# Optimization experiments

Measured on AMD Instinct MI355X. Metric: run time of the kernel, lower is better.

## Reference

```python
import jax, jax.numpy as jnp
import numpy as np

H, W = 128, 128
TANFOVX = 0.5
TANFOVY = 0.5
SCALE_MOD = 1.0
NEAR = 0.2
N = 2048


def setup_inputs() -> dict:
    key = jax.random.key(0)
    ks = jax.random.split(key, 6)
    # Gaussians in front of an identity camera looking down +z
    xy = jax.random.uniform(ks[0], (N, 2), minval=-1.5, maxval=1.5)
    z = jax.random.uniform(ks[1], (N, 1), minval=2.5, maxval=6.5)
    means3D = jnp.concatenate([xy, z], axis=1).astype(jnp.float32)
    opacities = jax.random.uniform(ks[2], (N, 1), minval=0.05, maxval=0.95)
    colors_precomp = jax.random.uniform(ks[3], (N, 3))
    scales = jax.random.uniform(ks[4], (N, 3), minval=0.01, maxval=0.06)
    rotations = jax.random.normal(ks[5], (N, 4))
    viewmatrix = jnp.eye(4, dtype=jnp.float32)  # world == camera frame
    bg = jnp.zeros((3,), dtype=jnp.float32)
    return dict(means3D=means3D, opacities=opacities,
                colors_precomp=colors_precomp, scales=scales,
                rotations=rotations, viewmatrix=viewmatrix, bg=bg)


def _quat_to_rot(q):
    # normalized quaternion (w, x, y, z) -> rotation matrix, as in the CUDA kernel
    q = q / jnp.linalg.norm(q, axis=-1, keepdims=True)
    w, x, y, z = q[:, 0], q[:, 1], q[:, 2], q[:, 3]
    return jnp.stack([
        jnp.stack([1 - 2 * (y * y + z * z), 2 * (x * y - w * z), 2 * (x * z + w * y)], -1),
        jnp.stack([2 * (x * y + w * z), 1 - 2 * (x * x + z * z), 2 * (y * z - w * x)], -1),
        jnp.stack([2 * (x * z - w * y), 2 * (y * z + w * x), 1 - 2 * (x * x + y * y)], -1),
    ], -2)  # [N,3,3]


def _forward(means3D, opacities, colors_precomp, scales, rotations, viewmatrix, bg):
    fx = W / (2.0 * TANFOVX)
    fy = H / (2.0 * TANFOVY)
    Rv = viewmatrix[:3, :3]
    tv = viewmatrix[:3, 3]
    pv = means3D @ Rv.T + tv            # view-space positions [N,3]
    x, y, z = pv[:, 0], pv[:, 1], pv[:, 2]
    zc = jnp.maximum(z, 1e-4)
    # frustum clamping of the EWA Jacobian, as in forward.cu
    tx = jnp.clip(x / zc, -1.3 * TANFOVX, 1.3 * TANFOVX) * zc
    ty = jnp.clip(y / zc, -1.3 * TANFOVY, 1.3 * TANFOVY) * zc
    zeros = jnp.zeros_like(zc)
    J = jnp.stack([
        jnp.stack([fx / zc, zeros, -fx * tx / (zc * zc)], -1),
        jnp.stack([zeros, fy / zc, -fy * ty / (zc * zc)], -1),
    ], -2)                               # [N,2,3]
    # 3D covariance Sigma = R S S^T R^T
    Rg = _quat_to_rot(rotations)
    M = Rg * (scales * SCALE_MOD)[:, None, :]
    Sigma = M @ jnp.swapaxes(M, -1, -2)  # [N,3,3]
    T2 = jnp.einsum('nij,jk->nik', J, Rv)
    cov2d = jnp.einsum('nij,njk,nlk->nil', T2, Sigma, T2)
    a = cov2d[:, 0, 0] + 0.3             # low-pass filter, as in CUDA
    b = cov2d[:, 0, 1]
    c = cov2d[:, 1, 1] + 0.3
    det = a * c - b * b
    valid = (det > 0) & (z > NEAR)
    inv_det = jnp.where(det != 0, 1.0 / det, 0.0)
    conA, conB, conC = c * inv_det, -b * inv_det, a * inv_det
    mid = 0.5 * (a + c)
    lam = mid + jnp.sqrt(jnp.maximum(mid * mid - det, 0.1))
    radii = jnp.where(valid, jnp.ceil(3.0 * jnp.sqrt(lam)), 0.0)
    # projected pixel-space means
    mx = fx * (x / zc) + 0.5 * (W - 1)
    my = fy * (y / zc) + 0.5 * (H - 1)

    # global front-to-back depth sort (CUDA sorts per tile; one tile here)
    order = jnp.argsort(z)
    mx_s, my_s = mx[order], my[order]
    A_s, B_s, C_s = conA[order], conB[order], conC[order]
    op_s = opacities[order, 0]
    z_s = z[order]
    col_s = colors_precomp[order]
    valid_s = valid[order]

    px = jnp.arange(W, dtype=means3D.dtype)
    py = jnp.arange(H, dtype=means3D.dtype)
    Dx = mx_s[None, :] - px[:, None]     # [W,N]
    Dy = my_s[None, :] - py[:, None]     # [H,N]
    # power = -0.5 (A dx^2 + C dy^2) - B dx dy, built [H,W,N]
    power = (-0.5 * A_s * Dx * Dx)[None, :, :] \
            + (-0.5 * C_s * Dy * Dy)[:, None, :] \
            - (B_s * Dx)[None, :, :] * Dy[:, None, :]
    alpha = jnp.minimum(0.99, op_s * jnp.exp(jnp.minimum(power, 0.0)))
    alpha = jnp.where((power <= 0.0) & valid_s & (alpha >= 1.0 / 255.0), alpha, 0.0)
    alpha = alpha.reshape(H * W, N)      # [HW,N], front-to-back order
    logt = jnp.log1p(-alpha)
    csum = jnp.cumsum(logt, axis=-1)
    T_excl = jnp.exp(csum - logt)        # exclusive transmittance prod_{j<i}(1-a_j)
    wgt = alpha * T_excl                 # compositing weights
    T_final = jnp.exp(csum[:, -1])
    color = jnp.einsum('pn,nc->cp', wgt, col_s).reshape(3, H, W) \
            + T_final.reshape(1, H, W) * bg[:, None, None]
    depth = (wgt * z_s[None, :]).sum(-1).reshape(H, W)
    alpha_img = (1.0 - T_final).reshape(H, W)
    return color, radii, depth, alpha_img


def reference(means3D, opacities, colors_precomp, scales, rotations, viewmatrix, bg):
    return _forward(means3D, opacities, colors_precomp, scales, rotations, viewmatrix, bg)
```

## Files before the change

### kernel.cpp

```cpp
#include <hip/hip_runtime.h>

#define NG    2048
#define IMG_W 128
#define IMG_H 128
#define NPIX  (IMG_W * IMG_H)
#define REC   12

__global__ __launch_bounds__(256) void prep_rank_kernel(
    const float* __restrict__ means,
    const float* __restrict__ opac,
    const float* __restrict__ cols,
    const float* __restrict__ scales,
    const float* __restrict__ rots,
    const float* __restrict__ vm4,
    float* __restrict__ s,
    float4* __restrict__ key4,
    float* __restrict__ radii_out)
{
    __shared__ __align__(16) float zl[NG];
    int tid = threadIdx.x;

    const double fx = 128.0, fy = 128.0;

    double R00 = vm4[0], R01 = vm4[1], R02 = vm4[2],  t0 = vm4[3];
    double R10 = vm4[4], R11 = vm4[5], R12 = vm4[6],  t1 = vm4[7];
    double R20 = vm4[8], R21 = vm4[9], R22 = vm4[10], t2 = vm4[11];

    for (int j = tid; j < NG; j += 256) {
        double zj = R20*means[3*j] + R21*means[3*j+1] + R22*means[3*j+2] + t2;
        zl[j] = (float)zj;
    }
    __syncthreads();

    int g = tid >> 4;
    int p = tid & 15;
    int i = blockIdx.x * 16 + g;
    float zi = zl[i];

    const float4* z4 = (const float4*)zl;
    int rank = 0;
    #pragma unroll 4
    for (int it = 0; it < 32; ++it) {
        int idx = it * 16 + p;
        float4 f = z4[idx];
        int j0 = idx * 4;
        rank += (f.x < zi) || (f.x == zi && (j0 + 0) < i);
        rank += (f.y < zi) || (f.y == zi && (j0 + 1) < i);
        rank += (f.z < zi) || (f.z == zi && (j0 + 2) < i);
        rank += (f.w < zi) || (f.w == zi && (j0 + 3) < i);
    }
    rank += __shfl_down(rank, 8, 16);
    rank += __shfl_down(rank, 4, 16);
    rank += __shfl_down(rank, 2, 16);
    rank += __shfl_down(rank, 1, 16);

    if (p != 0) return;

    double m0 = means[3*i+0], m1 = means[3*i+1], m2 = means[3*i+2];
    double x = R00*m0 + R01*m1 + R02*m2 + t0;
    double y = R10*m0 + R11*m1 + R12*m2 + t1;
    double z = R20*m0 + R21*m1 + R22*m2 + t2;

    double zc   = fmax(z, 1e-4);
    double invz = 1.0 / zc;
    const double limx = 1.3 * 0.5, limy = 1.3 * 0.5;
    double tx = fmin(limx, fmax(-limx, x * invz)) * zc;
    double ty = fmin(limy, fmax(-limy, y * invz)) * zc;

    double J00 = fx * invz, J02 = -fx * tx * invz * invz;
    double J11 = fy * invz, J12 = -fy * ty * invz * invz;

    double qw = rots[4*i+0], qx = rots[4*i+1], qy = rots[4*i+2], qz = rots[4*i+3];
    double qn = 1.0 / sqrt(qw*qw + qx*qx + qy*qy + qz*qz);
    qw *= qn; qx *= qn; qy *= qn; qz *= qn;

    double Rg00 = 1.0 - 2.0*(qy*qy + qz*qz), Rg01 = 2.0*(qx*qy - qw*qz), Rg02 = 2.0*(qx*qz + qw*qy);
    double Rg10 = 2.0*(qx*qy + qw*qz), Rg11 = 1.0 - 2.0*(qx*qx + qz*qz), Rg12 = 2.0*(qy*qz - qw*qx);
    double Rg20 = 2.0*(qx*qz - qw*qy), Rg21 = 2.0*(qy*qz + qw*qx), Rg22 = 1.0 - 2.0*(qx*qx + qy*qy);

    double s0 = scales[3*i+0], s1 = scales[3*i+1], s2 = scales[3*i+2];
    double M00 = Rg00*s0, M01 = Rg01*s1, M02 = Rg02*s2;
    double M10 = Rg10*s0, M11 = Rg11*s1, M12 = Rg12*s2;
    double M20 = Rg20*s0, M21 = Rg21*s1, M22 = Rg22*s2;

    double S00 = M00*M00 + M01*M01 + M02*M02;
    double S01 = M00*M10 + M01*M11 + M02*M12;
    double S02 = M00*M20 + M01*M21 + M02*M22;
    double S11 = M10*M10 + M11*M11 + M12*M12;
    double S12 = M10*M20 + M11*M21 + M12*M22;
    double S22 = M20*M20 + M21*M21 + M22*M22;

    double Ta0 = J00*R00 + J02*R20, Ta1 = J00*R01 + J02*R21, Ta2 = J00*R02 + J02*R22;
    double Tb0 = J11*R10 + J12*R20, Tb1 = J11*R11 + J12*R21, Tb2 = J11*R12 + J12*R22;

    double Ua0 = Ta0*S00 + Ta1*S01 + Ta2*S02;
    double Ua1 = Ta0*S01 + Ta1*S11 + Ta2*S12;
    double Ua2 = Ta0*S02 + Ta1*S12 + Ta2*S22;
    double Ub0 = Tb0*S00 + Tb1*S01 + Tb2*S02;
    double Ub1 = Tb0*S01 + Tb1*S11 + Tb2*S12;
    double Ub2 = Tb0*S02 + Tb1*S12 + Tb2*S22;
    double cov00 = Ua0*Ta0 + Ua1*Ta1 + Ua2*Ta2;
    double cov01 = Ua0*Tb0 + Ua1*Tb1 + Ua2*Tb2;
    double cov11 = Ub0*Tb0 + Ub1*Tb1 + Ub2*Tb2;

    double a = cov00 + 0.3;
    double b = cov01;
    double c = cov11 + 0.3;
    double det = a*c - b*b;
    bool valid = (det > 0.0) && (z > 0.2);
    double inv_det = (det != 0.0) ? (1.0 / det) : 0.0;
    double conA =  c * inv_det;
    double conB = -b * inv_det;
    double conC =  a * inv_det;
    double mid = 0.5 * (a + c);
    double lam = mid + sqrt(fmax(mid*mid - det, 0.1));
    float radii = valid ? (float)ceil(3.0 * sqrt(lam)) : 0.0f;

    double mx = fx * (x * invz) + 0.5 * (IMG_W - 1);
    double my = fy * (y * invz) + 0.5 * (IMG_H - 1);

    double op = valid ? (double)opac[i] : 0.0;

    double r2c = -1.0;
    if (op > 0.0) {
        double lnterm = log(255.0 * op);
        if (lnterm > 0.0) r2c = 2.0 * lnterm * lam * 1.0001 + 1e-3;
    }

    float* dst = s + (size_t)rank * REC;
    *(float4*)(dst)     = make_float4((float)mx, (float)my, (float)conA, (float)conB);
    *(float4*)(dst + 4) = make_float4((float)conC, (float)op, (float)z, cols[3*i+0]);
    *(float4*)(dst + 8) = make_float4(cols[3*i+1], cols[3*i+2], (float)r2c, 0.0f);
    key4[rank]   = make_float4((float)mx, (float)my, (float)r2c, 0.0f);
    radii_out[i] = radii;
}

__global__ __launch_bounds__(256) void composite_kernel(
    const float* __restrict__ s,
    const float4* __restrict__ key4,
    const float* __restrict__ bg,
    float* __restrict__ out)
{
    __shared__ float comb[4 * 64 * 5];

    int tid  = threadIdx.x;
    int lane = tid & 63;
    int w    = tid >> 6;
    int tile = blockIdx.x;
    int x0 = (tile & 15) * 8;
    int y0 = (tile >> 4) * 8;
    float x0f = (float)x0,       y0f = (float)y0;
    float x1f = (float)(x0 + 7), y1f = (float)(y0 + 7);

    int px = x0 + (lane & 7);
    int py = y0 + (lane >> 3);
    float fpx = (float)px, fpy = (float)py;
    int p = py * IMG_W + px;

    const int SEG = NG / 4;
    int segbase = w * SEG;

    unsigned long long m[8];
    unsigned pb = 0;
    #pragma unroll
    for (int c = 0; c < 8; ++c) {
        float4 k4 = key4[segbase + c * 64 + lane];
        float ddx = fmaxf(0.f, fmaxf(x0f - k4.x, k4.x - x1f));
        float ddy = fmaxf(0.f, fmaxf(y0f - k4.y, k4.y - y1f));
        bool pass = (ddx*ddx + ddy*ddy) <= k4.z;
        m[c] = __ballot(pass);
        pb |= pass ? (1u << c) : 0u;
    }

    float cr = 0.f, cg = 0.f, cb = 0.f, dep = 0.f, T = 1.f;

    #pragma unroll
    for (int c = 0; c < 8; ++c) {
        unsigned long long mm = m[c];
        if (!mm) continue;
        float4 a0 = make_float4(0.f,0.f,0.f,0.f);
        float4 a1 = a0;
        float2 a2 = make_float2(0.f,0.f);
        if ((pb >> c) & 1u) {
            const float* r = s + (size_t)(segbase + c * 64 + lane) * REC;
            a0 = *(const float4*)(r);
            a1 = *(const float4*)(r + 4);
            a2 = *(const float2*)(r + 8);
        }
        while (mm) {
            int b = __ffsll(mm) - 1;
            mm &= mm - 1;
            float mx = __shfl(a0.x, b);
            float my = __shfl(a0.y, b);
            float A  = __shfl(a0.z, b);
            float B  = __shfl(a0.w, b);
            float C  = __shfl(a1.x, b);
            float op = __shfl(a1.y, b);
            float dx = mx - fpx;
            float dy = my - fpy;
            float power = -0.5f * (A*dx*dx + C*dy*dy) - B*dx*dy;
            float al = fminf(0.99f, op * __expf(power));
            bool take = (power <= 0.0f) && (al >= (1.0f / 255.0f));
            if (__any(take)) {
                float gz = __shfl(a1.z, b);
                float gr = __shfl(a1.w, b);
                float gg = __shfl(a2.x, b);
                float gb = __shfl(a2.y, b);
                float wgt = take ? al * T : 0.0f;
                dep += wgt * gz;
                cr  += wgt * gr;
                cg  += wgt * gg;
                cb  += wgt * gb;
                if (take) T *= (1.0f - al);
            }
        }
    }

    int cb_base = (w * 64 + lane) * 5;
    comb[cb_base + 0] = cr;
    comb[cb_base + 1] = cg;
    comb[cb_base + 2] = cb;
    comb[cb_base + 3] = dep;
    comb[cb_base + 4] = T;
    __syncthreads();

    if (w == 0) {
        float CR = 0.f, CG = 0.f, CB = 0.f, DEP = 0.f, TT = 1.f;
        #pragma unroll
        for (int ww = 0; ww < 4; ++ww) {
            int b2 = (ww * 64 + lane) * 5;
            CR  += TT * comb[b2 + 0];
            CG  += TT * comb[b2 + 1];
            CB  += TT * comb[b2 + 2];
            DEP += TT * comb[b2 + 3];
            TT  *= comb[b2 + 4];
        }
        out[0*NPIX + p] = CR + TT * bg[0];
        out[1*NPIX + p] = CG + TT * bg[1];
        out[2*NPIX + p] = CB + TT * bg[2];
        out[3*NPIX + NG + p]        = DEP;
        out[3*NPIX + NG + NPIX + p] = 1.f - TT;
    }
}

extern "C" void kernel_launch(void* const* d_in, const int* in_sizes, int n_in,
                              void* d_out, int out_size, void* d_ws, size_t ws_size,
                              hipStream_t stream)
{
    const float* means = (const float*)d_in[0];
    const float* opac  = (const float*)d_in[1];
    const float* cols  = (const float*)d_in[2];
    const float* scl   = (const float*)d_in[3];
    const float* rot   = (const float*)d_in[4];
    const float* vm    = (const float*)d_in[5];
    const float* bg    = (const float*)d_in[6];
    float* out = (float*)d_out;

    float*  s    = (float*)d_ws;
    float4* key4 = (float4*)(s + NG * REC);

    prep_rank_kernel<<<NG / 16, 256, 0, stream>>>(
        means, opac, cols, scl, rot, vm, s, key4, out + 3 * NPIX);
    composite_kernel<<<NPIX / 64, 256, 0, stream>>>(s, key4, bg, out);
}
```

Measured before the change: 23.22 us.

## Fuse preprocessing and compositing into one per-tile kernel with local culling and sort

```diff
diff --git a/kernel.cpp b/kernel.cpp
--- a/kernel.cpp
+++ b/kernel.cpp
@@ -4,57 +4,24 @@
 #define IMG_W 128
 #define IMG_H 128
 #define NPIX  (IMG_W * IMG_H)
-#define REC   12
-
-__global__ __launch_bounds__(256) void prep_rank_kernel(
-    const float* __restrict__ means,
-    const float* __restrict__ opac,
-    const float* __restrict__ cols,
-    const float* __restrict__ scales,
-    const float* __restrict__ rots,
-    const float* __restrict__ vm4,
-    float* __restrict__ s,
-    float4* __restrict__ key4,
-    float* __restrict__ radii_out)
+#define KCAP  768
+
+struct PRec {
+    double mx, my, A, B, C, op, z, r2c;
+    float radii;
+};
+
+__device__ __forceinline__ void preprocess_g(
+    int i,
+    const float* __restrict__ means, const float* __restrict__ opac,
+    const float* __restrict__ scales, const float* __restrict__ rots,
+    const float* __restrict__ vm4, PRec& o)
 {
-    __shared__ __align__(16) float zl[NG];
-    int tid = threadIdx.x;
-
     const double fx = 128.0, fy = 128.0;
 
     double R00 = vm4[0], R01 = vm4[1], R02 = vm4[2],  t0 = vm4[3];
     double R10 = vm4[4], R11 = vm4[5], R12 = vm4[6],  t1 = vm4[7];
     double R20 = vm4[8], R21 = vm4[9], R22 = vm4[10], t2 = vm4[11];
-
-    for (int j = tid; j < NG; j += 256) {
-        double zj = R20*means[3*j] + R21*means[3*j+1] + R22*means[3*j+2] + t2;
-        zl[j] = (float)zj;
-    }
-    __syncthreads();
-
-    int g = tid >> 4;
-    int p = tid & 15;
-    int i = blockIdx.x * 16 + g;
-    float zi = zl[i];
-
-    const float4* z4 = (const float4*)zl;
-    int rank = 0;
-    #pragma unroll 4
-    for (int it = 0; it < 32; ++it) {
-        int idx = it * 16 + p;
-        float4 f = z4[idx];
-        int j0 = idx * 4;
-        rank += (f.x < zi) || (f.x == zi && (j0 + 0) < i);
-        rank += (f.y < zi) || (f.y == zi && (j0 + 1) < i);
-        rank += (f.z < zi) || (f.z == zi && (j0 + 2) < i);
-        rank += (f.w < zi) || (f.w == zi && (j0 + 3) < i);
-    }
-    rank += __shfl_down(rank, 8, 16);
-    rank += __shfl_down(rank, 4, 16);
-    rank += __shfl_down(rank, 2, 16);
-    rank += __shfl_down(rank, 1, 16);
-
-    if (p != 0) return;
 
     double m0 = means[3*i+0], m1 = means[3*i+1], m2 = means[3*i+2];
     double x = R00*m0 + R01*m1 + R02*m2 + t0;
@@ -109,111 +76,173 @@
     double det = a*c - b*b;
     bool valid = (det > 0.0) && (z > 0.2);
     double inv_det = (det != 0.0) ? (1.0 / det) : 0.0;
-    double conA =  c * inv_det;
-    double conB = -b * inv_det;
-    double conC =  a * inv_det;
     double mid = 0.5 * (a + c);
     double lam = mid + sqrt(fmax(mid*mid - det, 0.1));
-    float radii = valid ? (float)ceil(3.0 * sqrt(lam)) : 0.0f;
-
-    double mx = fx * (x * invz) + 0.5 * (IMG_W - 1);
-    double my = fy * (y * invz) + 0.5 * (IMG_H - 1);
 
     double op = valid ? (double)opac[i] : 0.0;
-
     double r2c = -1.0;
     if (op > 0.0) {
         double lnterm = log(255.0 * op);
         if (lnterm > 0.0) r2c = 2.0 * lnterm * lam * 1.0001 + 1e-3;
     }
 
-    float* dst = s + (size_t)rank * REC;
-    *(float4*)(dst)     = make_float4((float)mx, (float)my, (float)conA, (float)conB);
-    *(float4*)(dst + 4) = make_float4((float)conC, (float)op, (float)z, cols[3*i+0]);
-    *(float4*)(dst + 8) = make_float4(cols[3*i+1], cols[3*i+2], (float)r2c, 0.0f);
-    key4[rank]   = make_float4((float)mx, (float)my, (float)r2c, 0.0f);
-    radii_out[i] = radii;
+    o.mx  = fx * (x * invz) + 0.5 * (IMG_W - 1);
+    o.my  = fy * (y * invz) + 0.5 * (IMG_H - 1);
+    o.A   =  c * inv_det;
+    o.B   = -b * inv_det;
+    o.C   =  a * inv_det;
+    o.op  = op;
+    o.z   = z;
+    o.r2c = r2c;
+    o.radii = valid ? (float)ceil(3.0 * sqrt(lam)) : 0.0f;
 }
 
-__global__ __launch_bounds__(256) void composite_kernel(
-    const float* __restrict__ s,
-    const float4* __restrict__ key4,
+__global__ __launch_bounds__(256) void fused_raster_kernel(
+    const float* __restrict__ means,
+    const float* __restrict__ opac,
+    const float* __restrict__ cols,
+    const float* __restrict__ scales,
+    const float* __restrict__ rots,
+    const float* __restrict__ vm4,
     const float* __restrict__ bg,
     float* __restrict__ out)
 {
+    __shared__ unsigned short cand[NG];
+    __shared__ float recs[KCAP][10];
+    __shared__ float pz[KCAP];
+    __shared__ unsigned short pid[KCAP];
+    __shared__ unsigned short perm[KCAP];
     __shared__ float comb[4 * 64 * 5];
+    __shared__ int cntM, cntK;
 
     int tid  = threadIdx.x;
-    int lane = tid & 63;
-    int w    = tid >> 6;
     int tile = blockIdx.x;
     int x0 = (tile & 15) * 8;
     int y0 = (tile >> 4) * 8;
     float x0f = (float)x0,       y0f = (float)y0;
     float x1f = (float)(x0 + 7), y1f = (float)(y0 + 7);
 
+    if (tid == 0) { cntM = 0; cntK = 0; }
+    __syncthreads();
+
+    float fR00 = vm4[0], fR01 = vm4[1], fR02 = vm4[2],  ft0 = vm4[3];
+    float fR10 = vm4[4], fR11 = vm4[5], fR12 = vm4[6],  ft1 = vm4[7];
+    float fR20 = vm4[8], fR21 = vm4[9], fR22 = vm4[10], ft2 = vm4[11];
+
+    for (int g = tid; g < NG; g += 256) {
+        float m0 = means[3*g+0], m1 = means[3*g+1], m2 = means[3*g+2];
+        float x = fR00*m0 + fR01*m1 + fR02*m2 + ft0;
+        float y = fR10*m0 + fR11*m1 + fR12*m2 + ft1;
+        float z = fR20*m0 + fR21*m1 + fR22*m2 + ft2;
+        float zc = fmaxf(z, 1e-4f);
+        float invz = 1.0f / zc;
+        float xi = x * invz, yi = y * invz;
+        float mx = 128.f * xi + 63.5f;
+        float my = 128.f * yi + 63.5f;
+        float txc = fminf(0.65f, fmaxf(-0.65f, xi));
+        float tyc = fminf(0.65f, fmaxf(-0.65f, yi));
+        float J00 = 128.f * invz;
+        float J02 = -128.f * txc * invz;
+        float J12 = -128.f * tyc * invz;
+        float Ta0 = J00*fR00 + J02*fR20, Ta1 = J00*fR01 + J02*fR21, Ta2 = J00*fR02 + J02*fR22;
+        float Tb0 = J00*fR10 + J12*fR20, Tb1 = J00*fR11 + J12*fR21, Tb2 = J00*fR12 + J12*fR22;
+        float fro = Ta0*Ta0 + Ta1*Ta1 + Ta2*Ta2 + Tb0*Tb0 + Tb1*Tb1 + Tb2*Tb2;
+        float s0 = scales[3*g+0], s1 = scales[3*g+1], s2 = scales[3*g+2];
+        float smax2 = fmaxf(s0*s0, fmaxf(s1*s1, s2*s2));
+        float op = opac[g];
+        float lnterm = __logf(255.f * op);
+        bool maybe = false;
+        if (lnterm > 0.f) {
+            float lam_pf = fro * smax2 * 1.02f + 0.95f;
+            float r2 = 2.f * lnterm * lam_pf * 1.02f + 1.0f;
+            float ddx = fmaxf(0.f, fmaxf(x0f - mx, mx - x1f));
+            float ddy = fmaxf(0.f, fmaxf(y0f - my, my - y1f));
+            maybe = (ddx*ddx + ddy*ddy) <= r2;
+        }
+        if (maybe) {
+            int s = atomicAdd(&cntM, 1);
+            cand[s] = (unsigned short)g;
+        }
+    }
+
+    if (tid < 8) {
+        int i = tile * 8 + tid;
+        PRec o;
+        preprocess_g(i, means, opac, scales, rots, vm4, o);
+        out[3*NPIX + i] = o.radii;
+    }
+    __syncthreads();
+    int M = cntM;
+
+    for (int k = tid; k < M; k += 256) {
+        int gi = cand[k];
+        PRec o;
+        preprocess_g(gi, means, opac, scales, rots, vm4, o);
+        float fmx = (float)o.mx, fmy = (float)o.my, fr2 = (float)o.r2c;
+        float ddx = fmaxf(0.f, fmaxf(x0f - fmx, fmx - x1f));
+        float ddy = fmaxf(0.f, fmaxf(y0f - fmy, fmy - y1f));
+        if (ddx*ddx + ddy*ddy <= fr2) {
+            int s = atomicAdd(&cntK, 1);
+            if (s < KCAP) {
+                recs[s][0] = fmx;
+                recs[s][1] = fmy;
+                recs[s][2] = (float)o.A;
+                recs[s][3] = (float)o.B;
+                recs[s][4] = (float)o.C;
+                recs[s][5] = (float)o.op;
+                recs[s][6] = (float)o.z;
+                recs[s][7] = cols[3*gi+0];
+                recs[s][8] = cols[3*gi+1];
+                recs[s][9] = cols[3*gi+2];
+                pz[s]  = (float)o.z;
+                pid[s] = (unsigned short)gi;
+            }
+        }
+    }
+    __syncthreads();
+    int K = min(cntK, KCAP);
+
+    for (int r = tid; r < K; r += 256) {
+        float zr = pz[r];
+        int ir = pid[r];
+        int rank = 0;
+        for (int s2 = 0; s2 < K; ++s2)
+            rank += (pz[s2] < zr) || (pz[s2] == zr && pid[s2] < ir);
+        perm[rank] = (unsigned short)r;
+    }
+    __syncthreads();
+
+    int lane = tid & 63;
+    int w    = tid >> 6;
     int px = x0 + (lane & 7);
     int py = y0 + (lane >> 3);
     float fpx = (float)px, fpy = (float)py;
     int p = py * IMG_W + px;
 
-    const int SEG = NG / 4;
-    int segbase = w * SEG;
-
-    unsigned long long m[8];
-    unsigned pb = 0;
-    #pragma unroll
-    for (int c = 0; c < 8; ++c) {
-        float4 k4 = key4[segbase + c * 64 + lane];
-        float ddx = fmaxf(0.f, fmaxf(x0f - k4.x, k4.x - x1f));
-        float ddy = fmaxf(0.f, fmaxf(y0f - k4.y, k4.y - y1f));
-        bool pass = (ddx*ddx + ddy*ddy) <= k4.z;
-        m[c] = __ballot(pass);
-        pb |= pass ? (1u << c) : 0u;
-    }
+    int q = (K + 3) >> 2;
+    int rs = w * q;
+    int re = min(rs + q, K);
 
     float cr = 0.f, cg = 0.f, cb = 0.f, dep = 0.f, T = 1.f;
-
-    #pragma unroll
-    for (int c = 0; c < 8; ++c) {
-        unsigned long long mm = m[c];
-        if (!mm) continue;
-        float4 a0 = make_float4(0.f,0.f,0.f,0.f);
-        float4 a1 = a0;
-        float2 a2 = make_float2(0.f,0.f);
-        if ((pb >> c) & 1u) {
-            const float* r = s + (size_t)(segbase + c * 64 + lane) * REC;
-            a0 = *(const float4*)(r);
-            a1 = *(const float4*)(r + 4);
-            a2 = *(const float2*)(r + 8);
-        }
-        while (mm) {
-            int b = __ffsll(mm) - 1;
-            mm &= mm - 1;
-            float mx = __shfl(a0.x, b);
-            float my = __shfl(a0.y, b);
-            float A  = __shfl(a0.z, b);
-            float B  = __shfl(a0.w, b);
-            float C  = __shfl(a1.x, b);
-            float op = __shfl(a1.y, b);
-            float dx = mx - fpx;
-            float dy = my - fpy;
-            float power = -0.5f * (A*dx*dx + C*dy*dy) - B*dx*dy;
-            float al = fminf(0.99f, op * __expf(power));
-            bool take = (power <= 0.0f) && (al >= (1.0f / 255.0f));
-            if (__any(take)) {
-                float gz = __shfl(a1.z, b);
-                float gr = __shfl(a1.w, b);
-                float gg = __shfl(a2.x, b);
-                float gb = __shfl(a2.y, b);
-                float wgt = take ? al * T : 0.0f;
-                dep += wgt * gz;
-                cr  += wgt * gr;
-                cg  += wgt * gg;
-                cb  += wgt * gb;
-                if (take) T *= (1.0f - al);
-            }
-        }
+    for (int r = rs; r < re; ++r) {
+        int j = perm[r];
+        float mx = recs[j][0];
+        float my = recs[j][1];
+        float A  = recs[j][2];
+        float B  = recs[j][3];
+        float C  = recs[j][4];
+        float op = recs[j][5];
+        float dx = mx - fpx;
+        float dy = my - fpy;
+        float power = -0.5f * (A*dx*dx + C*dy*dy) - B*dx*dy;
+        float al = fminf(0.99f, op * __expf(power));
+        bool take = (power <= 0.0f) && (al >= (1.0f / 255.0f));
+        float wgt = take ? al * T : 0.0f;
+        dep += wgt * recs[j][6];
+        cr  += wgt * recs[j][7];
+        cg  += wgt * recs[j][8];
+        cb  += wgt * recs[j][9];
+        if (take) T *= (1.0f - al);
     }
 
     int cb_base = (w * 64 + lane) * 5;
@@ -256,10 +285,6 @@
     const float* bg    = (const float*)d_in[6];
     float* out = (float*)d_out;
 
-    float*  s    = (float*)d_ws;
-    float4* key4 = (float4*)(s + NG * REC);
-
-    prep_rank_kernel<<<NG / 16, 256, 0, stream>>>(
-        means, opac, cols, scl, rot, vm, s, key4, out + 3 * NPIX);
-    composite_kernel<<<NPIX / 64, 256, 0, stream>>>(s, key4, bg, out);
+    fused_raster_kernel<<<256, 256, 0, stream>>>(
+        means, opac, cols, scl, rot, vm, bg, out);
 }
```

Measured after the change: 24.26 us. 1.04x slower.
